# Optimization experiments

Hardware: AMD Instinct MI355X
Metric: run time of the kernel (lower is better)

The kernel has to match this reference:

```python
import jax, jax.numpy as jnp
import numpy as np

IN_FEATURES = 4096
OUT_FEATURES = 11008
BATCH = 2048


def setup_inputs() -> dict:
    key = jax.random.key(0)
    k1, k2, k3, k4 = jax.random.split(key, 4)
    # int8-range activations, stored as int32 for exact integer accumulation
    input = jax.random.randint(k1, (BATCH, IN_FEATURES), -127, 128, dtype=jnp.int32)
    # ternary weights in {-1, 0, 1}
    ternary_weight = jax.random.randint(k2, (OUT_FEATURES, IN_FEATURES), -1, 2, dtype=jnp.int32)
    weight_scale = jax.random.uniform(k3, (OUT_FEATURES, 1), dtype=jnp.float32, minval=0.01, maxval=0.1)
    bias = jax.random.normal(k4, (OUT_FEATURES,), dtype=jnp.float32) * 0.01
    return {"input": input, "ternary_weight": ternary_weight,
            "weight_scale": weight_scale, "bias": bias}


def reference(input, ternary_weight, weight_scale, bias):
    # Equivalent to the per-column add/sub loop: int32 accumulate of
    # input @ ternary_weight.T, since w in {-1,0,1}.
    acc = jnp.einsum('bi,oi->bo', input, ternary_weight)  # int32 [B, O]
    out = acc.astype(jnp.float32) * weight_scale.reshape(1, -1)
    out = out + bias
    return out
```

## Files before the change

### kernel.cpp

```cpp
#include <hip/hip_runtime.h>
#include <stdint.h>

#define BATCH   2048
#define KDIM    4096
#define NDIM    11008

#define BM 128
#define BN 256
#define BK 64
#define NT (KDIM / BK)
#define BUF_BYTES 24576
#define A_OFF 0
#define B_OFF 8192

typedef __attribute__((ext_vector_type(4))) int i32x4;

typedef const __attribute__((address_space(1))) char glob_char;
typedef __attribute__((address_space(3))) char lds_char;

__device__ __forceinline__ unsigned pack4(i32x4 v) {
  return  ((unsigned)v.x & 0xFFu)
        | (((unsigned)v.y & 0xFFu) << 8)
        | (((unsigned)v.z & 0xFFu) << 16)
        | (((unsigned)v.w)         << 24);
}

__global__ __launch_bounds__(256) void convert_i32_i8(const int* __restrict__ src,
                                                      unsigned* __restrict__ dst,
                                                      int n4) {
  int idx = blockIdx.x * 256 + threadIdx.x;
  if (idx >= n4) return;
  i32x4 v = ((const i32x4*)src)[idx];
  dst[idx] = pack4(v);
}

__global__ __launch_bounds__(512, 2) void ternary_gemm(const char* __restrict__ A8,
                                                       const char* __restrict__ B8,
                                                       const float* __restrict__ scale,
                                                       const float* __restrict__ bias,
                                                       float* __restrict__ out) {
  __shared__ char lds[3 * BUF_BYTES];

  const int tid  = threadIdx.x;
  const int wid  = tid >> 6;
  const int lane = tid & 63;

  const int nwg = gridDim.x;
  const int cpx = nwg >> 3;
  const int wg  = (blockIdx.x & 7) * cpx + (blockIdx.x >> 3);
  const int mt = wg & 15;
  const int nt = wg >> 4;
  const int arow0 = mt * BM;
  const int brow0 = nt * BN;

  const int wr = wid >> 2;
  const int wc = wid & 3;
  const int rsub = lane & 15;
  const int sgrp = lane >> 4;

  auto stage = [&](int bufi, int kt) {
    char* base = lds + bufi * BUF_BYTES;
    const int k0 = kt * BK;
    {
      const int row = tid >> 2;
      const int sl  = (tid & 3) ^ ((row >> 1) & 3);
      __builtin_amdgcn_global_load_lds(
          (glob_char*)(A8 + (size_t)(arow0 + row) * KDIM + k0 + sl * 16),
          (lds_char*)(base + A_OFF + wid * 1024), 16, 0, 0);
    }
#pragma unroll
    for (int c = 0; c < 2; ++c) {
      const int row = c * 128 + (tid >> 2);
      const int sl  = (tid & 3) ^ ((row >> 1) & 3);
      __builtin_amdgcn_global_load_lds(
          (glob_char*)(B8 + (size_t)(brow0 + row) * KDIM + k0 + sl * 16),
          (lds_char*)(base + B_OFF + c * 8192 + wid * 1024), 16, 0, 0);
    }
  };

  i32x4 acc[4][4];
#pragma unroll
  for (int m = 0; m < 4; ++m)
#pragma unroll
    for (int n = 0; n < 4; ++n)
      acc[m][n] = (i32x4){0, 0, 0, 0};

  stage(0, 0);
  stage(1, 1);
  asm volatile("s_waitcnt vmcnt(3)" ::: "memory");
  __builtin_amdgcn_s_barrier();
  __builtin_amdgcn_sched_barrier(0);

  int b0 = 0, b1 = 1, b2 = 2;

  for (int t = 0; t < NT; ++t) {
    const char* Ab = lds + b0 * BUF_BYTES;

    i32x4 af[4], bf[4];
#pragma unroll
    for (int m = 0; m < 4; ++m) {
      const int row = wr * 64 + m * 16 + rsub;
      const int p   = sgrp ^ ((row >> 1) & 3);
      af[m] = *(const i32x4*)(Ab + A_OFF + row * 64 + p * 16);
    }
#pragma unroll
    for (int n = 0; n < 4; ++n) {
      const int row = wc * 64 + n * 16 + rsub;
      const int p   = sgrp ^ ((row >> 1) & 3);
      bf[n] = *(const i32x4*)(Ab + B_OFF + row * 64 + p * 16);
    }

    int kt2 = t + 2;
    if (kt2 > NT - 1) kt2 = NT - 1;
    stage(b2, kt2);

    __builtin_amdgcn_s_barrier();

    __builtin_amdgcn_s_setprio(1);
#pragma unroll
    for (int m = 0; m < 4; ++m)
#pragma unroll
      for (int n = 0; n < 4; ++n)
        acc[m][n] = __builtin_amdgcn_mfma_i32_16x16x64_i8(af[m], bf[n], acc[m][n], 0, 0, 0);
    __builtin_amdgcn_s_setprio(0);

    asm volatile("s_waitcnt vmcnt(3)" ::: "memory");
    __builtin_amdgcn_s_barrier();
    __builtin_amdgcn_sched_barrier(0);

    const int tb = b0; b0 = b1; b1 = b2; b2 = tb;
  }

  const int crow = sgrp * 4;
#pragma unroll
  for (int n = 0; n < 4; ++n) {
    const int col = brow0 + wc * 64 + n * 16 + rsub;
    const float sc = scale[col];
    const float bs = bias[col];
#pragma unroll
    for (int m = 0; m < 4; ++m) {
      const int r0 = arow0 + wr * 64 + m * 16 + crow;
#pragma unroll
      for (int j = 0; j < 4; ++j) {
        out[(size_t)(r0 + j) * NDIM + col] = (float)acc[m][n][j] * sc + bs;
      }
    }
  }
}

extern "C" void kernel_launch(void* const* d_in, const int* in_sizes, int n_in,
                              void* d_out, int out_size, void* d_ws, size_t ws_size,
                              hipStream_t stream) {
  const int*   input  = (const int*)d_in[0];
  const int*   weight = (const int*)d_in[1];
  const float* scale  = (const float*)d_in[2];
  const float* bias   = (const float*)d_in[3];
  float*       out    = (float*)d_out;

  const size_t needA = (size_t)BATCH * KDIM;
  const size_t needB = (size_t)NDIM * KDIM;

  char* A8 = (char*)d_ws;
  char* B8 = A8 + needA;
  const int nA4 = (int)(needA / 4);
  const int nB4 = (int)(needB / 4);
  convert_i32_i8<<<(nA4 + 255) / 256, 256, 0, stream>>>(input, (unsigned*)A8, nA4);
  convert_i32_i8<<<(nB4 + 255) / 256, 256, 0, stream>>>(weight, (unsigned*)B8, nB4);

  const dim3 grid((BATCH / BM) * (NDIM / BN));
  const dim3 block(512);
  ternary_gemm<<<grid, block, 0, stream>>>(A8, B8, scale, bias, out);
  (void)ws_size; (void)n_in; (void)in_sizes; (void)out_size;
}
```

Measured before the change: 157.9 us.

## Switch to 32x32x32 i8 MFMA with 4-wave blocks and split-K register prefetch

Replaces the 16x16x64 int8 MFMA tiling with 32x32x32 MFMAs. Each of 4 waves now computes a 64x128 sub-tile, so blocks shrink from 512 to 256 threads. Each BK=64 tile is split into two K-halves: fragments for the second half and for the next tile are loaded from LDS while the MFMAs for the current half run, and the global-to-LDS staging is spread across the iteration. The goal is fewer LDS fragment reads per MFMA and better overlap of loads with compute. The cost is more waves-per-CU pressure from halved block size and more accumulator registers.

```diff
diff --git a/kernel.cpp b/kernel.cpp
--- a/kernel.cpp
+++ b/kernel.cpp
@@ -9,11 +9,14 @@
 #define BN 256
 #define BK 64
 #define NT (KDIM / BK)
-#define BUF_BYTES 24576
+#define ABYTES (BM * BK)
+#define BBYTES (BN * BK)
+#define BUF_BYTES (ABYTES + BBYTES)
 #define A_OFF 0
-#define B_OFF 8192
-
-typedef __attribute__((ext_vector_type(4))) int i32x4;
+#define B_OFF ABYTES
+
+typedef __attribute__((ext_vector_type(4)))  int i32x4;
+typedef __attribute__((ext_vector_type(16))) int i32x16;
 
 typedef const __attribute__((address_space(1))) char glob_char;
 typedef __attribute__((address_space(3))) char lds_char;
@@ -34,7 +37,7 @@
   dst[idx] = pack4(v);
 }
 
-__global__ __launch_bounds__(512, 2) void ternary_gemm(const char* __restrict__ A8,
+__global__ __launch_bounds__(256, 2) void ternary_gemm(const char* __restrict__ A8,
                                                        const char* __restrict__ B8,
                                                        const float* __restrict__ scale,
                                                        const float* __restrict__ bias,
@@ -44,6 +47,8 @@
   const int tid  = threadIdx.x;
   const int wid  = tid >> 6;
   const int lane = tid & 63;
+  const int l31  = lane & 31;
+  const int lhi  = lane >> 5;
 
   const int nwg = gridDim.x;
   const int cpx = nwg >> 3;
@@ -53,96 +58,127 @@
   const int arow0 = mt * BM;
   const int brow0 = nt * BN;
 
-  const int wr = wid >> 2;
-  const int wc = wid & 3;
-  const int rsub = lane & 15;
-  const int sgrp = lane >> 4;
-
-  auto stage = [&](int bufi, int kt) {
-    char* base = lds + bufi * BUF_BYTES;
-    const int k0 = kt * BK;
-    {
-      const int row = tid >> 2;
-      const int sl  = (tid & 3) ^ ((row >> 1) & 3);
-      __builtin_amdgcn_global_load_lds(
-          (glob_char*)(A8 + (size_t)(arow0 + row) * KDIM + k0 + sl * 16),
-          (lds_char*)(base + A_OFF + wid * 1024), 16, 0, 0);
-    }
-#pragma unroll
-    for (int c = 0; c < 2; ++c) {
-      const int row = c * 128 + (tid >> 2);
-      const int sl  = (tid & 3) ^ ((row >> 1) & 3);
-      __builtin_amdgcn_global_load_lds(
-          (glob_char*)(B8 + (size_t)(brow0 + row) * KDIM + k0 + sl * 16),
-          (lds_char*)(base + B_OFF + c * 8192 + wid * 1024), 16, 0, 0);
-    }
+  const int wr = wid >> 1;
+  const int wc = wid & 1;
+
+  const int srow = tid >> 2;
+  const int sslot = tid & 3;
+
+  auto stageA = [&](char* base, int kt, int r) {
+    const int row = r * 64 + srow;
+    const int sl  = sslot ^ ((row >> 1) & 3);
+    __builtin_amdgcn_global_load_lds(
+        (glob_char*)(A8 + (size_t)(arow0 + row) * KDIM + kt * BK + sl * 16),
+        (lds_char*)(base + A_OFF + r * 4096 + wid * 1024), 16, 0, 0);
   };
-
-  i32x4 acc[4][4];
-#pragma unroll
-  for (int m = 0; m < 4; ++m)
+  auto stageB = [&](char* base, int kt, int r) {
+    const int row = r * 64 + srow;
+    const int sl  = sslot ^ ((row >> 1) & 3);
+    __builtin_amdgcn_global_load_lds(
+        (glob_char*)(B8 + (size_t)(brow0 + row) * KDIM + kt * BK + sl * 16),
+        (lds_char*)(base + B_OFF + r * 4096 + wid * 1024), 16, 0, 0);
+  };
+
+  int offA[2][2], offB[4][2];
+#pragma unroll
+  for (int m = 0; m < 2; ++m)
+#pragma unroll
+    for (int kk = 0; kk < 2; ++kk) {
+      const int row = wr * 64 + m * 32 + l31;
+      const int p   = (kk * 2 + lhi) ^ ((row >> 1) & 3);
+      offA[m][kk] = A_OFF + row * 64 + p * 16;
+    }
+#pragma unroll
+  for (int n = 0; n < 4; ++n)
+#pragma unroll
+    for (int kk = 0; kk < 2; ++kk) {
+      const int row = wc * 128 + n * 32 + l31;
+      const int p   = (kk * 2 + lhi) ^ ((row >> 1) & 3);
+      offB[n][kk] = B_OFF + row * 64 + p * 16;
+    }
+
+  i32x16 acc[2][4];
+#pragma unroll
+  for (int m = 0; m < 2; ++m)
 #pragma unroll
     for (int n = 0; n < 4; ++n)
-      acc[m][n] = (i32x4){0, 0, 0, 0};
-
-  stage(0, 0);
-  stage(1, 1);
-  asm volatile("s_waitcnt vmcnt(3)" ::: "memory");
+      acc[m][n] = (i32x16)(0);
+
+  char* b0 = lds;
+  char* b1 = lds + BUF_BYTES;
+  char* b2 = lds + 2 * BUF_BYTES;
+
+  stageA(b0, 0, 0); stageA(b0, 0, 1);
+  stageB(b0, 0, 0); stageB(b0, 0, 1); stageB(b0, 0, 2); stageB(b0, 0, 3);
+  stageA(b1, 1, 0); stageA(b1, 1, 1);
+  stageB(b1, 1, 0); stageB(b1, 1, 1); stageB(b1, 1, 2); stageB(b1, 1, 3);
+  asm volatile("s_waitcnt vmcnt(6)" ::: "memory");
   __builtin_amdgcn_s_barrier();
-  __builtin_amdgcn_sched_barrier(0);
-
-  int b0 = 0, b1 = 1, b2 = 2;
+
+  i32x4 fa0[2], fb0[4], fa1[2], fb1[4];
+#pragma unroll
+  for (int m = 0; m < 2; ++m) fa0[m] = *(const i32x4*)(b0 + offA[m][0]);
+#pragma unroll
+  for (int n = 0; n < 4; ++n) fb0[n] = *(const i32x4*)(b0 + offB[n][0]);
 
   for (int t = 0; t < NT; ++t) {
-    const char* Ab = lds + b0 * BUF_BYTES;
-
-    i32x4 af[4], bf[4];
-#pragma unroll
-    for (int m = 0; m < 4; ++m) {
-      const int row = wr * 64 + m * 16 + rsub;
-      const int p   = sgrp ^ ((row >> 1) & 3);
-      af[m] = *(const i32x4*)(Ab + A_OFF + row * 64 + p * 16);
-    }
-#pragma unroll
-    for (int n = 0; n < 4; ++n) {
-      const int row = wc * 64 + n * 16 + rsub;
-      const int p   = sgrp ^ ((row >> 1) & 3);
-      bf[n] = *(const i32x4*)(Ab + B_OFF + row * 64 + p * 16);
-    }
-
-    int kt2 = t + 2;
-    if (kt2 > NT - 1) kt2 = NT - 1;
-    stage(b2, kt2);
-
+    const int kt2 = (t + 2 <= NT - 1) ? t + 2 : NT - 1;
+
+    stageA(b2, kt2, 0);
+    stageA(b2, kt2, 1);
+    stageB(b2, kt2, 0);
+#pragma unroll
+    for (int m = 0; m < 2; ++m) fa1[m] = *(const i32x4*)(b0 + offA[m][1]);
+#pragma unroll
+    for (int n = 0; n < 4; ++n) fb1[n] = *(const i32x4*)(b0 + offB[n][1]);
     __builtin_amdgcn_s_barrier();
 
     __builtin_amdgcn_s_setprio(1);
 #pragma unroll
-    for (int m = 0; m < 4; ++m)
+    for (int m = 0; m < 2; ++m)
 #pragma unroll
       for (int n = 0; n < 4; ++n)
-        acc[m][n] = __builtin_amdgcn_mfma_i32_16x16x64_i8(af[m], bf[n], acc[m][n], 0, 0, 0);
+        acc[m][n] = __builtin_amdgcn_mfma_i32_32x32x32_i8(fa0[m], fb0[n], acc[m][n], 0, 0, 0);
     __builtin_amdgcn_s_setprio(0);
 
-    asm volatile("s_waitcnt vmcnt(3)" ::: "memory");
+    stageB(b2, kt2, 1);
+    stageB(b2, kt2, 2);
+    stageB(b2, kt2, 3);
+    asm volatile("s_waitcnt vmcnt(6)" ::: "memory");
     __builtin_amdgcn_s_barrier();
+
+    if (t < NT - 1) {
+#pragma unroll
+      for (int m = 0; m < 2; ++m) fa0[m] = *(const i32x4*)(b1 + offA[m][0]);
+#pragma unroll
+      for (int n = 0; n < 4; ++n) fb0[n] = *(const i32x4*)(b1 + offB[n][0]);
+    }
+
+    __builtin_amdgcn_s_setprio(1);
+#pragma unroll
+    for (int m = 0; m < 2; ++m)
+#pragma unroll
+      for (int n = 0; n < 4; ++n)
+        acc[m][n] = __builtin_amdgcn_mfma_i32_32x32x32_i8(fa1[m], fb1[n], acc[m][n], 0, 0, 0);
+    __builtin_amdgcn_s_setprio(0);
+    __builtin_amdgcn_s_barrier();
+
+    char* tb = b0; b0 = b1; b1 = b2; b2 = tb;
     __builtin_amdgcn_sched_barrier(0);
-
-    const int tb = b0; b0 = b1; b1 = b2; b2 = tb;
   }
 
-  const int crow = sgrp * 4;
 #pragma unroll
   for (int n = 0; n < 4; ++n) {
-    const int col = brow0 + wc * 64 + n * 16 + rsub;
+    const int col = brow0 + wc * 128 + n * 32 + l31;
     const float sc = scale[col];
     const float bs = bias[col];
 #pragma unroll
-    for (int m = 0; m < 4; ++m) {
-      const int r0 = arow0 + wr * 64 + m * 16 + crow;
-#pragma unroll
-      for (int j = 0; j < 4; ++j) {
-        out[(size_t)(r0 + j) * NDIM + col] = (float)acc[m][n][j] * sc + bs;
+    for (int m = 0; m < 2; ++m) {
+      const int r0 = arow0 + wr * 64 + m * 32 + 4 * lhi;
+#pragma unroll
+      for (int reg = 0; reg < 16; ++reg) {
+        const int row = r0 + (reg & 3) + 8 * (reg >> 2);
+        out[(size_t)row * NDIM + col] = (float)acc[m][n][reg] * sc + bs;
       }
     }
   }
@@ -168,7 +204,7 @@
   convert_i32_i8<<<(nB4 + 255) / 256, 256, 0, stream>>>(weight, (unsigned*)B8, nB4);
 
   const dim3 grid((BATCH / BM) * (NDIM / BN));
-  const dim3 block(512);
+  const dim3 block(256);
   ternary_gemm<<<grid, block, 0, stream>>>(A8, B8, scale, bias, out);
   (void)ws_size; (void)n_in; (void)in_sizes; (void)out_size;
 }
```

Measured after the change: 163.9 us. 3.8% more time.

## Split main loop into four interleaved LDS-read/stage/MFMA phases with more barriers

Applied to the files above, without the earlier changes.

Restructures the K-loop into four sub-phases. Each phase loads only part of the A/B fragments from LDS, issues one slice of the next-tile global-to-LDS staging, and runs a 2x2 block of MFMAs. This aims to overlap LDS reads, global prefetch and matrix math more finely and to cut register pressure. It also precomputes global and LDS addresses once, and raises launch_bounds to request 4 waves per SIMD. The trade-off is roughly eight barriers per iteration instead of two. Occupancy is still capped by LDS, since 72KB per block of 512 threads likely allows only two blocks per CU.

```diff
diff --git a/kernel.cpp b/kernel.cpp
--- a/kernel.cpp
+++ b/kernel.cpp
@@ -9,9 +9,11 @@
 #define BN 256
 #define BK 64
 #define NT (KDIM / BK)
-#define BUF_BYTES 24576
+#define ABYTES (BM * BK)
+#define BBYTES (BN * BK)
+#define BUF_BYTES (ABYTES + BBYTES)
 #define A_OFF 0
-#define B_OFF 8192
+#define B_OFF ABYTES
 
 typedef __attribute__((ext_vector_type(4))) int i32x4;
 
@@ -34,7 +36,7 @@
   dst[idx] = pack4(v);
 }
 
-__global__ __launch_bounds__(512, 2) void ternary_gemm(const char* __restrict__ A8,
+__global__ __launch_bounds__(512, 4) void ternary_gemm(const char* __restrict__ A8,
                                                        const char* __restrict__ B8,
                                                        const float* __restrict__ scale,
                                                        const float* __restrict__ bias,
@@ -58,25 +60,35 @@
   const int rsub = lane & 15;
   const int sgrp = lane >> 4;
 
-  auto stage = [&](int bufi, int kt) {
-    char* base = lds + bufi * BUF_BYTES;
-    const int k0 = kt * BK;
-    {
-      const int row = tid >> 2;
-      const int sl  = (tid & 3) ^ ((row >> 1) & 3);
-      __builtin_amdgcn_global_load_lds(
-          (glob_char*)(A8 + (size_t)(arow0 + row) * KDIM + k0 + sl * 16),
-          (lds_char*)(base + A_OFF + wid * 1024), 16, 0, 0);
-    }
-#pragma unroll
-    for (int c = 0; c < 2; ++c) {
-      const int row = c * 128 + (tid >> 2);
-      const int sl  = (tid & 3) ^ ((row >> 1) & 3);
-      __builtin_amdgcn_global_load_lds(
-          (glob_char*)(B8 + (size_t)(brow0 + row) * KDIM + k0 + sl * 16),
-          (lds_char*)(base + B_OFF + c * 8192 + wid * 1024), 16, 0, 0);
-    }
+  const int srow  = tid >> 2;
+  const int sslot = (tid & 3) ^ ((srow >> 1) & 3);
+  const char* gA  = A8 + (size_t)(arow0 + srow) * KDIM + sslot * 16;
+  const char* gB0 = B8 + (size_t)(brow0 + srow) * KDIM + sslot * 16;
+  const char* gB1 = B8 + (size_t)(brow0 + 128 + srow) * KDIM + sslot * 16;
+
+  auto stageA = [&](int bufo, int kt) {
+    __builtin_amdgcn_global_load_lds((glob_char*)(gA + kt * BK),
+        (lds_char*)(lds + bufo + A_OFF + wid * 1024), 16, 0, 0);
   };
+  auto stageB = [&](int bufo, int kt, int r) {
+    const char* g = (r == 0) ? gB0 : gB1;
+    __builtin_amdgcn_global_load_lds((glob_char*)(g + kt * BK),
+        (lds_char*)(lds + bufo + B_OFF + r * 8192 + wid * 1024), 16, 0, 0);
+  };
+
+  int offA[4], offB[4];
+#pragma unroll
+  for (int m = 0; m < 4; ++m) {
+    const int row = wr * 64 + m * 16 + rsub;
+    const int p   = sgrp ^ ((row >> 1) & 3);
+    offA[m] = A_OFF + row * 64 + p * 16;
+  }
+#pragma unroll
+  for (int n = 0; n < 4; ++n) {
+    const int row = wc * 64 + n * 16 + rsub;
+    const int p   = sgrp ^ ((row >> 1) & 3);
+    offB[n] = B_OFF + row * 64 + p * 16;
+  }
 
   i32x4 acc[4][4];
 #pragma unroll
@@ -85,50 +97,67 @@
     for (int n = 0; n < 4; ++n)
       acc[m][n] = (i32x4){0, 0, 0, 0};
 
-  stage(0, 0);
-  stage(1, 1);
+  int cur = 0, nxt = BUF_BYTES, pf = 2 * BUF_BYTES;
+
+  stageB(cur, 0, 0); stageB(cur, 0, 1); stageA(cur, 0);
+  stageB(nxt, 1, 0); stageB(nxt, 1, 1); stageA(nxt, 1);
   asm volatile("s_waitcnt vmcnt(3)" ::: "memory");
   __builtin_amdgcn_s_barrier();
-  __builtin_amdgcn_sched_barrier(0);
-
-  int b0 = 0, b1 = 1, b2 = 2;
 
   for (int t = 0; t < NT; ++t) {
-    const char* Ab = lds + b0 * BUF_BYTES;
-
-    i32x4 af[4], bf[4];
-#pragma unroll
-    for (int m = 0; m < 4; ++m) {
-      const int row = wr * 64 + m * 16 + rsub;
-      const int p   = sgrp ^ ((row >> 1) & 3);
-      af[m] = *(const i32x4*)(Ab + A_OFF + row * 64 + p * 16);
-    }
-#pragma unroll
-    for (int n = 0; n < 4; ++n) {
-      const int row = wc * 64 + n * 16 + rsub;
-      const int p   = sgrp ^ ((row >> 1) & 3);
-      bf[n] = *(const i32x4*)(Ab + B_OFF + row * 64 + p * 16);
-    }
-
-    int kt2 = t + 2;
-    if (kt2 > NT - 1) kt2 = NT - 1;
-    stage(b2, kt2);
-
-    __builtin_amdgcn_s_barrier();
-
-    __builtin_amdgcn_s_setprio(1);
-#pragma unroll
-    for (int m = 0; m < 4; ++m)
-#pragma unroll
-      for (int n = 0; n < 4; ++n)
-        acc[m][n] = __builtin_amdgcn_mfma_i32_16x16x64_i8(af[m], bf[n], acc[m][n], 0, 0, 0);
-    __builtin_amdgcn_s_setprio(0);
+    const int kt2 = (t + 2 < NT) ? t + 2 : NT - 1;
+
+    i32x4 a0, a1, a2, a3, b0, b1, b2, b3;
+
+    a0 = *(const i32x4*)(lds + cur + offA[0]);
+    a1 = *(const i32x4*)(lds + cur + offA[1]);
+    b0 = *(const i32x4*)(lds + cur + offB[0]);
+    b1 = *(const i32x4*)(lds + cur + offB[1]);
+    stageB(pf, kt2, 0);
+    __builtin_amdgcn_s_barrier();
+    __builtin_amdgcn_s_setprio(1);
+    acc[0][0] = __builtin_amdgcn_mfma_i32_16x16x64_i8(a0, b0, acc[0][0], 0, 0, 0);
+    acc[0][1] = __builtin_amdgcn_mfma_i32_16x16x64_i8(a0, b1, acc[0][1], 0, 0, 0);
+    acc[1][0] = __builtin_amdgcn_mfma_i32_16x16x64_i8(a1, b0, acc[1][0], 0, 0, 0);
+    acc[1][1] = __builtin_amdgcn_mfma_i32_16x16x64_i8(a1, b1, acc[1][1], 0, 0, 0);
+    __builtin_amdgcn_s_setprio(0);
+    __builtin_amdgcn_s_barrier();
+
+    b2 = *(const i32x4*)(lds + cur + offB[2]);
+    b3 = *(const i32x4*)(lds + cur + offB[3]);
+    stageB(pf, kt2, 1);
+    __builtin_amdgcn_s_barrier();
+    __builtin_amdgcn_s_setprio(1);
+    acc[0][2] = __builtin_amdgcn_mfma_i32_16x16x64_i8(a0, b2, acc[0][2], 0, 0, 0);
+    acc[0][3] = __builtin_amdgcn_mfma_i32_16x16x64_i8(a0, b3, acc[0][3], 0, 0, 0);
+    acc[1][2] = __builtin_amdgcn_mfma_i32_16x16x64_i8(a1, b2, acc[1][2], 0, 0, 0);
+    acc[1][3] = __builtin_amdgcn_mfma_i32_16x16x64_i8(a1, b3, acc[1][3], 0, 0, 0);
+    __builtin_amdgcn_s_setprio(0);
+    __builtin_amdgcn_s_barrier();
+
+    a2 = *(const i32x4*)(lds + cur + offA[2]);
+    a3 = *(const i32x4*)(lds + cur + offA[3]);
+    stageA(pf, kt2);
+    __builtin_amdgcn_s_barrier();
+    __builtin_amdgcn_s_setprio(1);
+    acc[2][2] = __builtin_amdgcn_mfma_i32_16x16x64_i8(a2, b2, acc[2][2], 0, 0, 0);
+    acc[2][3] = __builtin_amdgcn_mfma_i32_16x16x64_i8(a2, b3, acc[2][3], 0, 0, 0);
+    acc[3][2] = __builtin_amdgcn_mfma_i32_16x16x64_i8(a3, b2, acc[3][2], 0, 0, 0);
+    acc[3][3] = __builtin_amdgcn_mfma_i32_16x16x64_i8(a3, b3, acc[3][3], 0, 0, 0);
+    __builtin_amdgcn_s_setprio(0);
+    __builtin_amdgcn_s_barrier();
 
     asm volatile("s_waitcnt vmcnt(3)" ::: "memory");
     __builtin_amdgcn_s_barrier();
-    __builtin_amdgcn_sched_barrier(0);
-
-    const int tb = b0; b0 = b1; b1 = b2; b2 = tb;
+    __builtin_amdgcn_s_setprio(1);
+    acc[2][0] = __builtin_amdgcn_mfma_i32_16x16x64_i8(a2, b0, acc[2][0], 0, 0, 0);
+    acc[2][1] = __builtin_amdgcn_mfma_i32_16x16x64_i8(a2, b1, acc[2][1], 0, 0, 0);
+    acc[3][0] = __builtin_amdgcn_mfma_i32_16x16x64_i8(a3, b0, acc[3][0], 0, 0, 0);
+    acc[3][1] = __builtin_amdgcn_mfma_i32_16x16x64_i8(a3, b1, acc[3][1], 0, 0, 0);
+    __builtin_amdgcn_s_setprio(0);
+    __builtin_amdgcn_s_barrier();
+
+    const int tb = cur; cur = nxt; nxt = pf; pf = tb;
   }
 
   const int crow = sgrp * 4;
```

Result: no change. 156.2 us (-1.1%).
